# Performance work log

Hardware: AMD Instinct MI355X
Metric: run time of the kernel (lower is better)

## Reference

```python
import jax, jax.numpy as jnp
import numpy as np

H, DH = 8, 64           # heads, dim_head
SCALE = DH ** -0.5


def setup_inputs() -> dict:
    key = jax.random.key(0)
    ks = jax.random.split(key, 8)
    b, f, n, dim = 16, 8, 256, 512
    inner = H * DH
    w = lambda k, s: jax.random.normal(k, s, jnp.float32) * 0.02
    return {
        "x": jax.random.normal(ks[0], (b, f * n, dim), jnp.float32),
        "external": jax.random.normal(ks[1], (b, 1, dim), jnp.float32),
        "Wq": w(ks[2], (dim, inner)), "bq": jnp.zeros((inner,), jnp.float32),
        "Wk": w(ks[3], (dim, inner)), "bk": jnp.zeros((inner,), jnp.float32),
        "Wv": w(ks[4], (dim, inner)), "bv": jnp.zeros((inner,), jnp.float32),
        "Wo": w(ks[5], (inner, dim)), "bo": jnp.zeros((dim,), jnp.float32),
        "f": f,
    }


def reference(x, external, Wq, bq, Wk, bk, Wv, bv, Wo, bo, f):
    b, N, dim = x.shape          # N = f * n
    n = N // f
    xa = jnp.concatenate([external, x], axis=1)          # (b, N+1, dim)

    def proj(W, bias):
        t = xa @ W + bias                                # (b, N+1, H*DH)
        # 'b n (h d) -> (b h) n d'
        return t.reshape(b, N + 1, H, DH).transpose(0, 2, 1, 3).reshape(b * H, N + 1, DH)

    q = proj(Wq, bq) * SCALE
    k = proj(Wk, bk)
    v = proj(Wv, bv)

    def split_local(t):
        ext = jnp.repeat(t[:, :1], f, axis=0)            # (b*H*f, 1, DH)  'b n d -> (b r) n d'
        loc = t[:, 1:].reshape(b * H * f, n, DH)         # 'b (f n) d -> (b f) n d'
        return jnp.concatenate([ext, loc], axis=1)       # (b*H*f, n+1, DH)

    q_, k_, v_ = split_local(q), split_local(k), split_local(v)

    att = jax.nn.softmax(jnp.einsum('bid,bjd->bij', q_, k_), axis=-1)
    out = jnp.einsum('bij,bjd->bid', att, v_)            # (b*H*f, n+1, DH)

    # external token output: '(b h r) d -> b r (h d)' then take r == 1
    ext_out = out[:, 0].reshape(b, H, f, DH).transpose(0, 2, 1, 3).reshape(b, f, H * DH)
    ext_out = ext_out[:, 1:2]                            # (b, 1, H*DH)

    # local outputs: '(b f) n d -> b (f n) d' then '(b h) n d -> b n (h d)'
    main = out[:, 1:].reshape(b, H, N, DH).transpose(0, 2, 1, 3).reshape(b, N, H * DH)

    return main @ Wo + bo, ext_out @ Wo + bo
```

## Files before the change

kernel.cpp:

```cpp
#include <hip/hip_runtime.h>
#include <stdint.h>

#define ATT_SCALE 0.125f

typedef __attribute__((ext_vector_type(8))) short bhalf8;
typedef __attribute__((ext_vector_type(4))) float floatx4;
typedef __attribute__((ext_vector_type(16))) float floatx16;
typedef __attribute__((ext_vector_type(8))) unsigned short ush8;

__device__ __forceinline__ unsigned short f2bf(float f) {
  union { float f; unsigned int u; } v; v.f = f;
  unsigned int r = v.u + 0x7fffu + ((v.u >> 16) & 1u);
  return (unsigned short)(r >> 16);
}
__device__ __forceinline__ float bf2f(unsigned short u) {
  union { unsigned int u; float f; } v; v.u = ((unsigned int)u) << 16;
  return v.f;
}
__device__ __forceinline__ unsigned int pk2(float a, float b) {
  unsigned int r;
  asm("v_cvt_pk_bf16_f32 %0, %1, %2" : "=v"(r) : "v"(a), "v"(b));
  return r;
}
__device__ __forceinline__ void glds16(const void* g, void* l) {
  __builtin_amdgcn_global_load_lds(
      (__attribute__((address_space(1))) void*)g,
      (__attribute__((address_space(3))) void*)l, 16, 0, 0);
}

__global__ __launch_bounds__(256) void k_conv_x(const float* __restrict__ x,
                                                unsigned short* __restrict__ out) {
  int i = blockIdx.x * 256 + threadIdx.x;
  float4 v = ((const float4*)x)[i];
  ((uint2*)out)[i] = make_uint2(pk2(v.x, v.y), pk2(v.z, v.w));
}

__global__ __launch_bounds__(256) void k_conv_w(
    const float* __restrict__ Wq, const float* __restrict__ Wk,
    const float* __restrict__ Wv, const float* __restrict__ Wo,
    const float* __restrict__ bq, const float* __restrict__ bk, const float* __restrict__ bv,
    unsigned short* __restrict__ Wqkvt, unsigned short* __restrict__ Wot,
    float* __restrict__ biasqkv) {
  int idx = blockIdx.x * 256 + threadIdx.x;
  {
    int nn = idx >> 9, k = idx & 511;
    const float* W = (nn < 512) ? Wq : ((nn < 1024) ? Wk : Wv);
    int n = nn & 511;
    Wqkvt[idx] = f2bf(W[k * 512 + n]);
  }
  if (idx < 512 * 512) {
    int n = idx >> 9, k = idx & 511;
    Wot[idx] = f2bf(Wo[k * 512 + n]);
  }
  if (idx < 1536) {
    biasqkv[idx] = (idx < 512) ? bq[idx] : ((idx < 1024) ? bk[idx - 512] : bv[idx - 1024]);
  }
}

__global__ __launch_bounds__(256) void k_ext_qkv(
    const float* __restrict__ ext,
    const float* __restrict__ Wq, const float* __restrict__ Wk, const float* __restrict__ Wv,
    const float* __restrict__ bq, const float* __restrict__ bk, const float* __restrict__ bv,
    float* __restrict__ EQKV) {
  int b = blockIdx.x / 6, c = blockIdx.x % 6;
  int nn = c * 256 + threadIdx.x;
  __shared__ float xs[512];
  xs[threadIdx.x] = ext[b * 512 + threadIdx.x];
  xs[256 + threadIdx.x] = ext[b * 512 + 256 + threadIdx.x];
  __syncthreads();
  const float* W; const float* bias; float scale = 1.f; int n;
  if (nn < 512)      { W = Wq; bias = bq; n = nn;        scale = ATT_SCALE; }
  else if (nn < 1024){ W = Wk; bias = bk; n = nn - 512; }
  else               { W = Wv; bias = bv; n = nn - 1024; }
  float acc = 0.f;
  #pragma unroll 8
  for (int k = 0; k < 512; ++k) acc += xs[k] * W[k * 512 + n];
  EQKV[b * 1536 + nn] = (acc + bias[n]) * scale;
}

template <int EPI>
__global__ __launch_bounds__(256, 2) void k_gemm(
    const unsigned short* __restrict__ A, const unsigned short* __restrict__ B,
    const float* __restrict__ bias, void* __restrict__ Cptr, int N, int nbn) {
  __shared__ __align__(16) unsigned short S[16384];
  int tid = threadIdx.x, lane = tid & 63, wv = tid >> 6;
  int lo = lane & 15, hi = lane >> 4;
  int waveM = wv >> 1, waveN = wv & 1;

  int nwg = gridDim.x;
  int wg = (blockIdx.x & 7) * (nwg >> 3) + (blockIdx.x >> 3);
  int bm = wg / nbn, bn = wg % nbn;

  const unsigned short* Ab = A + (size_t)bm * 128 * 512;
  const unsigned short* Bb = B + (size_t)bn * 128 * 512;
  unsigned short* lA = S;
  unsigned short* lB = S + 8192;

  floatx4 acc[4][4];
  #pragma unroll
  for (int m = 0; m < 4; ++m)
    #pragma unroll
    for (int n = 0; n < 4; ++n) acc[m][n] = floatx4{0.f, 0.f, 0.f, 0.f};

  for (int kt = 0; kt < 8; ++kt) {
    __syncthreads();
    #pragma unroll
    for (int i = 0; i < 4; ++i) {
      int chunk = i * 256 + tid;
      int row = chunk >> 3, slot = chunk & 7;
      glds16(Ab + (size_t)row * 512 + kt * 64 + ((slot ^ (row & 7)) << 3),
             lA + (size_t)(i * 256 + wv * 64) * 8);
    }
    #pragma unroll
    for (int i = 0; i < 4; ++i) {
      int chunk = i * 256 + tid;
      int row = chunk >> 3, slot = chunk & 7;
      glds16(Bb + (size_t)row * 512 + kt * 64 + ((slot ^ (row & 7)) << 3),
             lB + (size_t)(i * 256 + wv * 64) * 8);
    }
    __syncthreads();

    bhalf8 af[4][2], bf4[4][2];
    #pragma unroll
    for (int m = 0; m < 4; ++m) {
      int row = waveM * 64 + m * 16 + lo;
      #pragma unroll
      for (int ks = 0; ks < 2; ++ks)
        af[m][ks] = *(const bhalf8*)(lA + (size_t)row * 64 + (((ks * 4 + hi) ^ (row & 7)) << 3));
    }
    #pragma unroll
    for (int n = 0; n < 4; ++n) {
      int row = waveN * 64 + n * 16 + lo;
      #pragma unroll
      for (int ks = 0; ks < 2; ++ks)
        bf4[n][ks] = *(const bhalf8*)(lB + (size_t)row * 64 + (((ks * 4 + hi) ^ (row & 7)) << 3));
    }
    #pragma unroll
    for (int m = 0; m < 4; ++m)
      #pragma unroll
      for (int n = 0; n < 4; ++n) {
        acc[m][n] = __builtin_amdgcn_mfma_f32_16x16x32_bf16(af[m][0], bf4[n][0], acc[m][n], 0, 0, 0);
        acc[m][n] = __builtin_amdgcn_mfma_f32_16x16x32_bf16(af[m][1], bf4[n][1], acc[m][n], 0, 0, 0);
      }
  }

  #pragma unroll
  for (int m = 0; m < 4; ++m) {
    int row0 = bm * 128 + waveM * 64 + m * 16 + hi * 4;
    #pragma unroll
    for (int n = 0; n < 4; ++n) {
      int col = bn * 128 + waveN * 64 + n * 16 + lo;
      float bb = bias[col];
      #pragma unroll
      for (int r = 0; r < 4; ++r) {
        float v = acc[m][n][r] + bb;
        if constexpr (EPI == 0) {
          if (col < 512) v *= ATT_SCALE;
          ((unsigned short*)Cptr)[(size_t)(row0 + r) * N + col] = f2bf(v);
        } else {
          ((float*)Cptr)[(size_t)(row0 + r) * N + col] = v;
        }
      }
    }
  }
}

#define VTC 296
__global__ __launch_bounds__(512, 4) void k_attn(
    const unsigned short* __restrict__ QKV,
    const float* __restrict__ EQKV,
    unsigned short* __restrict__ mainb) {
  __shared__ __align__(16) unsigned short Ks[288 * 64];
  __shared__ __align__(16) unsigned short Vt[64 * VTC];
  int g = blockIdx.x;
  int b = g >> 6, h = (g >> 3) & 7, j = g & 7;
  int tid = threadIdx.x, lane = tid & 63, wv = tid >> 6;
  int ql = lane & 31, hb = lane >> 5;
  const size_t rowbase = (size_t)b * 2048 + (size_t)j * 256;
  const unsigned short* Kg = QKV + rowbase * 1536 + 512 + h * 64;
  const unsigned short* Vg = QKV + rowbase * 1536 + 1024 + h * 64;

  int qbase = wv * 32;
  const unsigned short* qp = QKV + (rowbase + qbase + ql) * 1536 + h * 64 + hb * 8;
  bhalf8 qf[4];
  #pragma unroll
  for (int c = 0; c < 4; ++c) qf[c] = *(const bhalf8*)(qp + c * 16);

  {
    ush8 z8 = {0, 0, 0, 0, 0, 0, 0, 0};
    for (int c = tid; c < (64 * VTC) / 8; c += 512) ((ush8*)Vt)[c] = z8;
  }
  __syncthreads();

  {
    int keybase = 1 + wv * 32;
    #pragma unroll
    for (int i = 0; i < 4; ++i) {
      int key = keybase + i * 8 + (lane >> 3);
      int slot = lane & 7;
      const unsigned short* src =
          Kg + (size_t)(key - 1) * 1536 + (((slot * 16) ^ ((key & 7) << 4)) >> 1);
      glds16(src, &Ks[(size_t)(keybase + i * 8) * 64]);
    }
  }
  for (int c = tid; c < 2048; c += 512) {
    int key = 1 + (c & 255), d0 = (c >> 8) * 8;
    ush8 vv = *(const ush8*)(Vg + (size_t)(key - 1) * 1536 + d0);
    #pragma unroll
    for (int u = 0; u < 8; ++u) Vt[(d0 + u) * VTC + key] = vv[u];
  }
  if (wv == 0) {
    Ks[lane] = f2bf(EQKV[b * 1536 + 512 + h * 64 + lane]);
    Vt[lane * VTC] = f2bf(EQKV[b * 1536 + 1024 + h * 64 + lane]);
  }
  __syncthreads();

  floatx16 o0, o1;
  #pragma unroll
  for (int i = 0; i < 16; ++i) { o0[i] = 0.f; o1[i] = 0.f; }
  float m = -1e30f, lsum = 0.f;

  #pragma unroll
  for (int t = 0; t < 9; ++t) {
    floatx16 s;
    #pragma unroll
    for (int i = 0; i < 16; ++i) s[i] = 0.f;
    int key = t * 32 + ql;
    __builtin_amdgcn_s_setprio(1);
    #pragma unroll
    for (int c = 0; c < 4; ++c) {
      bhalf8 kf = *(const bhalf8*)((const char*)Ks + key * 128 +
                                   ((c * 32 + hb * 16) ^ ((key & 7) << 4)));
      s = __builtin_amdgcn_mfma_f32_32x32x16_bf16(kf, qf[c], s, 0, 0, 0);
    }
    __builtin_amdgcn_s_setprio(0);
    if (t == 8) {
      #pragma unroll
      for (int r = 0; r < 16; ++r) {
        if (r == 0) { if (hb != 0) s[0] = -1e30f; }
        else s[r] = -1e30f;
      }
    }
    float mt = s[0];
    #pragma unroll
    for (int r = 1; r < 16; ++r) mt = fmaxf(mt, s[r]);
    mt = fmaxf(mt, __shfl_xor(mt, 32, 64));
    if (!__all(mt - m <= 8.f)) {
      float mnew = fmaxf(m, mt);
      float corr = __expf(m - mnew);
      lsum *= corr;
      #pragma unroll
      for (int r = 0; r < 16; ++r) { o0[r] *= corr; o1[r] *= corr; }
      m = mnew;
    }
    float p[16]; float ts = 0.f;
    #pragma unroll
    for (int r = 0; r < 16; ++r) { p[r] = __expf(s[r] - m); ts += p[r]; }
    lsum += ts;
    unsigned int pk[8], qk[8];
    #pragma unroll
    for (int i = 0; i < 8; ++i) pk[i] = pk2(p[2 * i], p[2 * i + 1]);
    #pragma unroll
    for (int i = 0; i < 8; ++i) qk[i] = __shfl_xor(pk[i], 32, 64);
    bhalf8 f0, f1;
    unsigned int* f0u = (unsigned int*)&f0;
    unsigned int* f1u = (unsigned int*)&f1;
    if (hb == 0) {
      f0u[0] = pk[0]; f0u[1] = pk[1]; f0u[2] = qk[0]; f0u[3] = qk[1];
      f1u[0] = pk[4]; f1u[1] = pk[5]; f1u[2] = qk[4]; f1u[3] = qk[5];
    } else {
      f0u[0] = qk[2]; f0u[1] = qk[3]; f0u[2] = pk[2]; f0u[3] = pk[3];
      f1u[0] = qk[6]; f1u[1] = qk[7]; f1u[2] = pk[6]; f1u[3] = pk[7];
    }
    {
      const char* vb0 = (const char*)Vt + ((0 * 32 + ql) * VTC + t * 32 + hb * 8) * 2;
      bhalf8 v0 = *(const bhalf8*)vb0;
      bhalf8 v1 = *(const bhalf8*)(vb0 + 32);
      const char* vb1 = (const char*)Vt + ((1 * 32 + ql) * VTC + t * 32 + hb * 8) * 2;
      bhalf8 w0 = *(const bhalf8*)vb1;
      bhalf8 w1 = *(const bhalf8*)(vb1 + 32);
      __builtin_amdgcn_s_setprio(1);
      o0 = __builtin_amdgcn_mfma_f32_32x32x16_bf16(v0, f0, o0, 0, 0, 0);
      o0 = __builtin_amdgcn_mfma_f32_32x32x16_bf16(v1, f1, o0, 0, 0, 0);
      o1 = __builtin_amdgcn_mfma_f32_32x32x16_bf16(w0, f0, o1, 0, 0, 0);
      o1 = __builtin_amdgcn_mfma_f32_32x32x16_bf16(w1, f1, o1, 0, 0, 0);
      __builtin_amdgcn_s_setprio(0);
    }
  }

  lsum += __shfl_xor(lsum, 32, 64);
  float rinv = 1.f / lsum;
  __syncthreads();
  char* ob = (char*)(Ks + wv * 2048);
  #pragma unroll
  for (int dt = 0; dt < 2; ++dt) {
    #pragma unroll
    for (int i = 0; i < 8; ++i) {
      int d0 = dt * 32 + ((2 * i) & 3) + 8 * (i >> 1) + 4 * hb;
      float a = (dt ? o1[2 * i] : o0[2 * i]) * rinv;
      float c = (dt ? o1[2 * i + 1] : o0[2 * i + 1]) * rinv;
      *(unsigned int*)(ob + ql * 128 + ((d0 * 2) ^ ((ql & 7) << 4))) = pk2(a, c);
    }
  }
  #pragma unroll
  for (int i = 0; i < 4; ++i) {
    int chunk = i * 64 + lane;
    int q = chunk >> 3, slot = chunk & 7;
    bhalf8 vv = *(const bhalf8*)(ob + q * 128 + ((slot * 16) ^ ((q & 7) << 4)));
    *(bhalf8*)(mainb + (rowbase + qbase + q) * 512 + h * 64 + slot * 8) = vv;
  }
}

__global__ __launch_bounds__(256) void k_ext_attn(
    const unsigned short* __restrict__ QKV, const float* __restrict__ EQKV,
    float* __restrict__ extpre) {
  int b = blockIdx.x >> 3, h = blockIdx.x & 7;
  int tid = threadIdx.x, lane = tid & 63, wv = tid >> 6;
  __shared__ float qs[64];
  __shared__ float ps[257];
  __shared__ float red[8];
  __shared__ float acc4[4][64];
  if (tid < 64) qs[tid] = EQKV[b * 1536 + h * 64 + tid];
  __syncthreads();
  const size_t base = (size_t)b * 2048 + 256;
  float sc[2] = {-1e30f, -1e30f};
  #pragma unroll
  for (int it = 0; it < 2; ++it) {
    int key = tid + it * 256;
    if (key < 257) {
      float s = 0.f;
      if (key == 0) {
        const float* kr = EQKV + b * 1536 + 512 + h * 64;
        #pragma unroll 8
        for (int d = 0; d < 64; ++d) s += qs[d] * kr[d];
      } else {
        const unsigned short* kr = QKV + (base + key - 1) * 1536 + 512 + h * 64;
        #pragma unroll
        for (int c = 0; c < 8; ++c) {
          ush8 kv = *(const ush8*)(kr + c * 8);
          #pragma unroll
          for (int u = 0; u < 8; ++u) s += qs[c * 8 + u] * bf2f(kv[u]);
        }
      }
      sc[it] = s;
    }
  }
  float lmax = fmaxf(sc[0], sc[1]);
  for (int d = 1; d < 64; d <<= 1) lmax = fmaxf(lmax, __shfl_xor(lmax, d, 64));
  if (lane == 0) red[wv] = lmax;
  __syncthreads();
  float M = fmaxf(fmaxf(red[0], red[1]), fmaxf(red[2], red[3]));
  float lsum = 0.f;
  #pragma unroll
  for (int it = 0; it < 2; ++it) {
    int key = tid + it * 256;
    if (key < 257) { float p = __expf(sc[it] - M); ps[key] = p; lsum += p; }
  }
  for (int d = 1; d < 64; d <<= 1) lsum += __shfl_xor(lsum, d, 64);
  if (lane == 0) red[4 + wv] = lsum;
  __syncthreads();
  float S = red[4] + red[5] + red[6] + red[7];
  int d = tid & 63, part = tid >> 6;
  float acc = 0.f;
  for (int key = part; key < 257; key += 4) {
    float vv = (key == 0) ? EQKV[b * 1536 + 1024 + h * 64 + d]
                          : bf2f(QKV[(base + key - 1) * 1536 + 1024 + h * 64 + d]);
    acc += ps[key] * vv;
  }
  acc4[part][d] = acc;
  __syncthreads();
  if (tid < 64) {
    float r = (acc4[0][tid] + acc4[1][tid] + acc4[2][tid] + acc4[3][tid]) / S;
    extpre[b * 512 + h * 64 + tid] = r;
  }
}

__global__ __launch_bounds__(256) void k_ext_out(
    const float* __restrict__ extpre, const float* __restrict__ Wo,
    const float* __restrict__ bo, float* __restrict__ out) {
  int b = blockIdx.x, half = blockIdx.y;
  int n = half * 256 + threadIdx.x;
  __shared__ float xs[512];
  xs[threadIdx.x] = extpre[b * 512 + threadIdx.x];
  xs[256 + threadIdx.x] = extpre[b * 512 + 256 + threadIdx.x];
  __syncthreads();
  float acc = bo[n];
  #pragma unroll 8
  for (int k = 0; k < 512; ++k) acc += xs[k] * Wo[k * 512 + n];
  out[16777216 + b * 512 + n] = acc;
}

extern "C" void kernel_launch(void* const* d_in, const int* in_sizes, int n_in,
                              void* d_out, int out_size, void* d_ws, size_t ws_size,
                              hipStream_t stream) {
  (void)in_sizes; (void)n_in; (void)out_size; (void)ws_size;
  const float* x   = (const float*)d_in[0];
  const float* ext = (const float*)d_in[1];
  const float* Wq  = (const float*)d_in[2];
  const float* bq  = (const float*)d_in[3];
  const float* Wk  = (const float*)d_in[4];
  const float* bk  = (const float*)d_in[5];
  const float* Wv  = (const float*)d_in[6];
  const float* bv  = (const float*)d_in[7];
  const float* Wo  = (const float*)d_in[8];
  const float* bo  = (const float*)d_in[9];
  float* out = (float*)d_out;

  char* ws = (char*)d_ws;
  size_t off = 0;
  auto take = [&](size_t bytes) { char* p = ws + off; off += (bytes + 255) & ~(size_t)255; return p; };
  unsigned short* Xbf    = (unsigned short*)take((size_t)32768 * 512 * 2);
  unsigned short* Wqkvt  = (unsigned short*)take((size_t)1536 * 512 * 2);
  unsigned short* Wot    = (unsigned short*)take((size_t)512 * 512 * 2);
  float*          biasqkv= (float*)take(1536 * 4);
  float*          EQKV   = (float*)take(16 * 1536 * 4);
  unsigned short* QKVb   = (unsigned short*)take((size_t)32768 * 1536 * 2);
  unsigned short* mainb  = (unsigned short*)take((size_t)32768 * 512 * 2);
  float*          extpre = (float*)take(16 * 512 * 4);

  k_conv_x<<<16384, 256, 0, stream>>>(x, Xbf);
  k_conv_w<<<3072, 256, 0, stream>>>(Wq, Wk, Wv, Wo, bq, bk, bv, Wqkvt, Wot, biasqkv);
  k_ext_qkv<<<96, 256, 0, stream>>>(ext, Wq, Wk, Wv, bq, bk, bv, EQKV);
  k_gemm<0><<<3072, 256, 0, stream>>>(Xbf, Wqkvt, biasqkv, QKVb, 1536, 12);
  k_attn<<<1024, 512, 0, stream>>>(QKVb, EQKV, mainb);
  k_ext_attn<<<128, 256, 0, stream>>>(QKVb, EQKV, extpre);
  k_gemm<1><<<1024, 256, 0, stream>>>(mainb, Wot, bo, out, 512, 4);
  k_ext_out<<<dim3(16, 2), 256, 0, stream>>>(extpre, Wo, bo, out);
}
```

Measured before the change: 220.7 us.

## Fuse fp32-to-bf16 conversion of x into QKV GEMM; seed attention with external token

Removes the separate k_conv_x pass and its bf16 staging buffer: the QKV GEMM now loads fp32 x tiles straight into LDS with an XOR swizzle and converts them to bf16 in registers before the MFMAs. The attention kernel drops the extra 32-key tile that held the external token. It now computes the external-token score directly in fp32 and uses it to initialise the running max, sum and output, which also removes the Vt zeroing pass and a barrier. The trade-off is that fp32 A tiles double the A-side LDS footprint and load traffic per GEMM tile, and the conversions are repeated by each of the 12 column tiles, which could lower occupancy.

```diff
diff --git a/kernel.cpp b/kernel.cpp
--- a/kernel.cpp
+++ b/kernel.cpp
@@ -26,13 +26,6 @@
   __builtin_amdgcn_global_load_lds(
       (__attribute__((address_space(1))) void*)g,
       (__attribute__((address_space(3))) void*)l, 16, 0, 0);
-}
-
-__global__ __launch_bounds__(256) void k_conv_x(const float* __restrict__ x,
-                                                unsigned short* __restrict__ out) {
-  int i = blockIdx.x * 256 + threadIdx.x;
-  float4 v = ((const float4*)x)[i];
-  ((uint2*)out)[i] = make_uint2(pk2(v.x, v.y), pk2(v.z, v.w));
 }
 
 __global__ __launch_bounds__(256) void k_conv_w(
@@ -78,10 +71,96 @@
   EQKV[b * 1536 + nn] = (acc + bias[n]) * scale;
 }
 
-template <int EPI>
-__global__ __launch_bounds__(256, 2) void k_gemm(
+__global__ __launch_bounds__(256, 2) void k_gemm_qkv(
+    const float* __restrict__ X, const unsigned short* __restrict__ B,
+    const float* __restrict__ bias, unsigned short* __restrict__ C) {
+  __shared__ __align__(16) float Af[8192];
+  __shared__ __align__(16) unsigned short Bs[8192];
+  int tid = threadIdx.x, lane = tid & 63, wv = tid >> 6;
+  int lo = lane & 15, hi = lane >> 4;
+  int waveM = wv >> 1, waveN = wv & 1;
+
+  int nwg = gridDim.x;
+  int wg = (blockIdx.x & 7) * (nwg >> 3) + (blockIdx.x >> 3);
+  int bm = wg / 12, bn = wg % 12;
+
+  const float* Xb = X + (size_t)bm * 128 * 512;
+  const unsigned short* Bb = B + (size_t)bn * 128 * 512;
+
+  floatx4 acc[4][4];
+  #pragma unroll
+  for (int m = 0; m < 4; ++m)
+    #pragma unroll
+    for (int n = 0; n < 4; ++n) acc[m][n] = floatx4{0.f, 0.f, 0.f, 0.f};
+
+  for (int kt = 0; kt < 8; ++kt) {
+    __syncthreads();
+    #pragma unroll
+    for (int i = 0; i < 8; ++i) {
+      int chunk = i * 256 + tid;
+      int row = chunk >> 4, slot = chunk & 15;
+      glds16(Xb + (size_t)row * 512 + kt * 64 + ((slot ^ (row & 15)) << 2),
+             Af + (size_t)(i * 256 + wv * 64) * 4);
+    }
+    #pragma unroll
+    for (int i = 0; i < 4; ++i) {
+      int chunk = i * 256 + tid;
+      int row = chunk >> 3, slot = chunk & 7;
+      glds16(Bb + (size_t)row * 512 + kt * 64 + ((slot ^ (row & 7)) << 3),
+             Bs + (size_t)(i * 256 + wv * 64) * 8);
+    }
+    __syncthreads();
+
+    bhalf8 af[4][2], bf4[4][2];
+    #pragma unroll
+    for (int m = 0; m < 4; ++m) {
+      int row = waveM * 64 + m * 16 + lo;
+      #pragma unroll
+      for (int ks = 0; ks < 2; ++ks) {
+        int j0 = (ks * 4 + hi) * 2;
+        float4 fa = *(const float4*)(Af + (size_t)row * 64 + ((j0 ^ (row & 15)) << 2));
+        float4 fb = *(const float4*)(Af + (size_t)row * 64 + (((j0 + 1) ^ (row & 15)) << 2));
+        unsigned int* w = (unsigned int*)&af[m][ks];
+        w[0] = pk2(fa.x, fa.y); w[1] = pk2(fa.z, fa.w);
+        w[2] = pk2(fb.x, fb.y); w[3] = pk2(fb.z, fb.w);
+      }
+    }
+    #pragma unroll
+    for (int n = 0; n < 4; ++n) {
+      int row = waveN * 64 + n * 16 + lo;
+      #pragma unroll
+      for (int ks = 0; ks < 2; ++ks)
+        bf4[n][ks] = *(const bhalf8*)(Bs + (size_t)row * 64 + (((ks * 4 + hi) ^ (row & 7)) << 3));
+    }
+    #pragma unroll
+    for (int m = 0; m < 4; ++m)
+      #pragma unroll
+      for (int n = 0; n < 4; ++n) {
+        acc[m][n] = __builtin_amdgcn_mfma_f32_16x16x32_bf16(af[m][0], bf4[n][0], acc[m][n], 0, 0, 0);
+        acc[m][n] = __builtin_amdgcn_mfma_f32_16x16x32_bf16(af[m][1], bf4[n][1], acc[m][n], 0, 0, 0);
+      }
+  }
+
+  #pragma unroll
+  for (int m = 0; m < 4; ++m) {
+    int row0 = bm * 128 + waveM * 64 + m * 16 + hi * 4;
+    #pragma unroll
+    for (int n = 0; n < 4; ++n) {
+      int col = bn * 128 + waveN * 64 + n * 16 + lo;
+      float bb = bias[col];
+      #pragma unroll
+      for (int r = 0; r < 4; ++r) {
+        float v = acc[m][n][r] + bb;
+        if (col < 512) v *= ATT_SCALE;
+        C[(size_t)(row0 + r) * 1536 + col] = f2bf(v);
+      }
+    }
+  }
+}
+
+__global__ __launch_bounds__(256, 2) void k_gemm_out(
     const unsigned short* __restrict__ A, const unsigned short* __restrict__ B,
-    const float* __restrict__ bias, void* __restrict__ Cptr, int N, int nbn) {
+    const float* __restrict__ bias, float* __restrict__ C) {
   __shared__ __align__(16) unsigned short S[16384];
   int tid = threadIdx.x, lane = tid & 63, wv = tid >> 6;
   int lo = lane & 15, hi = lane >> 4;
@@ -89,7 +168,7 @@
 
   int nwg = gridDim.x;
   int wg = (blockIdx.x & 7) * (nwg >> 3) + (blockIdx.x >> 3);
-  int bm = wg / nbn, bn = wg % nbn;
+  int bm = wg / 4, bn = wg % 4;
 
   const unsigned short* Ab = A + (size_t)bm * 128 * 512;
   const unsigned short* Bb = B + (size_t)bn * 128 * 512;
@@ -152,15 +231,8 @@
       int col = bn * 128 + waveN * 64 + n * 16 + lo;
       float bb = bias[col];
       #pragma unroll
-      for (int r = 0; r < 4; ++r) {
-        float v = acc[m][n][r] + bb;
-        if constexpr (EPI == 0) {
-          if (col < 512) v *= ATT_SCALE;
-          ((unsigned short*)Cptr)[(size_t)(row0 + r) * N + col] = f2bf(v);
-        } else {
-          ((float*)Cptr)[(size_t)(row0 + r) * N + col] = v;
-        }
-      }
+      for (int r = 0; r < 4; ++r)
+        C[(size_t)(row0 + r) * 512 + col] = acc[m][n][r] + bb;
     }
   }
 }
@@ -170,8 +242,9 @@
     const unsigned short* __restrict__ QKV,
     const float* __restrict__ EQKV,
     unsigned short* __restrict__ mainb) {
-  __shared__ __align__(16) unsigned short Ks[288 * 64];
+  __shared__ __align__(16) unsigned short Ks[256 * 64];
   __shared__ __align__(16) unsigned short Vt[64 * VTC];
+  __shared__ float kx[64], vx[64];
   int g = blockIdx.x;
   int b = g >> 6, h = (g >> 3) & 7, j = g & 7;
   int tid = threadIdx.x, lane = tid & 63, wv = tid >> 6;
@@ -187,41 +260,46 @@
   for (int c = 0; c < 4; ++c) qf[c] = *(const bhalf8*)(qp + c * 16);
 
   {
-    ush8 z8 = {0, 0, 0, 0, 0, 0, 0, 0};
-    for (int c = tid; c < (64 * VTC) / 8; c += 512) ((ush8*)Vt)[c] = z8;
-  }
-  __syncthreads();
-
-  {
-    int keybase = 1 + wv * 32;
+    int keybase = wv * 32;
     #pragma unroll
     for (int i = 0; i < 4; ++i) {
       int key = keybase + i * 8 + (lane >> 3);
       int slot = lane & 7;
       const unsigned short* src =
-          Kg + (size_t)(key - 1) * 1536 + (((slot * 16) ^ ((key & 7) << 4)) >> 1);
+          Kg + (size_t)key * 1536 + (((slot * 16) ^ ((key & 7) << 4)) >> 1);
       glds16(src, &Ks[(size_t)(keybase + i * 8) * 64]);
     }
   }
   for (int c = tid; c < 2048; c += 512) {
-    int key = 1 + (c & 255), d0 = (c >> 8) * 8;
-    ush8 vv = *(const ush8*)(Vg + (size_t)(key - 1) * 1536 + d0);
+    int key = c & 255, d0 = (c >> 8) * 8;
+    ush8 vv = *(const ush8*)(Vg + (size_t)key * 1536 + d0);
     #pragma unroll
     for (int u = 0; u < 8; ++u) Vt[(d0 + u) * VTC + key] = vv[u];
   }
-  if (wv == 0) {
-    Ks[lane] = f2bf(EQKV[b * 1536 + 512 + h * 64 + lane]);
-    Vt[lane * VTC] = f2bf(EQKV[b * 1536 + 1024 + h * 64 + lane]);
-  }
-  __syncthreads();
-
+  if (tid < 64) {
+    kx[tid] = EQKV[b * 1536 + 512 + h * 64 + tid];
+    vx[tid] = EQKV[b * 1536 + 1024 + h * 64 + tid];
+  }
+  __syncthreads();
+
+  float part = 0.f;
+  #pragma unroll
+  for (int c = 0; c < 4; ++c)
+    #pragma unroll
+    for (int u = 0; u < 8; ++u)
+      part += bf2f((unsigned short)qf[c][u]) * kx[c * 16 + hb * 8 + u];
+  float m = part + __shfl_xor(part, 32, 64);
+  float lsum = 1.f;
   floatx16 o0, o1;
   #pragma unroll
-  for (int i = 0; i < 16; ++i) { o0[i] = 0.f; o1[i] = 0.f; }
-  float m = -1e30f, lsum = 0.f;
-
-  #pragma unroll
-  for (int t = 0; t < 9; ++t) {
+  for (int i = 0; i < 8; ++i) {
+    int d0 = ((2 * i) & 3) + 8 * (i >> 1) + 4 * hb;
+    o0[2 * i] = vx[d0];       o0[2 * i + 1] = vx[d0 + 1];
+    o1[2 * i] = vx[32 + d0];  o1[2 * i + 1] = vx[32 + d0 + 1];
+  }
+
+  #pragma unroll
+  for (int t = 0; t < 8; ++t) {
     floatx16 s;
     #pragma unroll
     for (int i = 0; i < 16; ++i) s[i] = 0.f;
@@ -234,13 +312,6 @@
       s = __builtin_amdgcn_mfma_f32_32x32x16_bf16(kf, qf[c], s, 0, 0, 0);
     }
     __builtin_amdgcn_s_setprio(0);
-    if (t == 8) {
-      #pragma unroll
-      for (int r = 0; r < 16; ++r) {
-        if (r == 0) { if (hb != 0) s[0] = -1e30f; }
-        else s[r] = -1e30f;
-      }
-    }
     float mt = s[0];
     #pragma unroll
     for (int r = 1; r < 16; ++r) mt = fmaxf(mt, s[r]);
@@ -409,7 +480,6 @@
   char* ws = (char*)d_ws;
   size_t off = 0;
   auto take = [&](size_t bytes) { char* p = ws + off; off += (bytes + 255) & ~(size_t)255; return p; };
-  unsigned short* Xbf    = (unsigned short*)take((size_t)32768 * 512 * 2);
   unsigned short* Wqkvt  = (unsigned short*)take((size_t)1536 * 512 * 2);
   unsigned short* Wot    = (unsigned short*)take((size_t)512 * 512 * 2);
   float*          biasqkv= (float*)take(1536 * 4);
@@ -418,12 +488,11 @@
   unsigned short* mainb  = (unsigned short*)take((size_t)32768 * 512 * 2);
   float*          extpre = (float*)take(16 * 512 * 4);
 
-  k_conv_x<<<16384, 256, 0, stream>>>(x, Xbf);
   k_conv_w<<<3072, 256, 0, stream>>>(Wq, Wk, Wv, Wo, bq, bk, bv, Wqkvt, Wot, biasqkv);
   k_ext_qkv<<<96, 256, 0, stream>>>(ext, Wq, Wk, Wv, bq, bk, bv, EQKV);
-  k_gemm<0><<<3072, 256, 0, stream>>>(Xbf, Wqkvt, biasqkv, QKVb, 1536, 12);
+  k_gemm_qkv<<<3072, 256, 0, stream>>>(x, Wqkvt, biasqkv, QKVb);
   k_attn<<<1024, 512, 0, stream>>>(QKVb, EQKV, mainb);
   k_ext_attn<<<128, 256, 0, stream>>>(QKVb, EQKV, extpre);
-  k_gemm<1><<<1024, 256, 0, stream>>>(mainb, Wot, bo, out, 512, 4);
+  k_gemm_out<<<1024, 256, 0, stream>>>(mainb, Wot, bo, out);
   k_ext_out<<<dim3(16, 2), 256, 0, stream>>>(extpre, Wo, bo, out);
 }
```

New measurement: 224.6 us. About the same (+1.8%).

## Handle external key/value token analytically instead of a ninth padded tile

Applied to the files above, without the earlier changes.

The external token's key and value are no longer written into shared memory as key slot 0, which had forced a ninth, mostly masked 32-key MFMA tile. The kernel now computes the query-external score with a scalar dot product in fp32 and uses it to seed the online softmax state, with the running max set to that score, the sum set to one and the output initialised to the external value. It also removes the Vt zero-fill pass and one block barrier. The risk is that the hardcoded accumulator layout mapping for the output seed must match the MFMA output layout exactly.

```diff
diff --git a/kernel.cpp b/kernel.cpp
--- a/kernel.cpp
+++ b/kernel.cpp
@@ -170,8 +170,9 @@
     const unsigned short* __restrict__ QKV,
     const float* __restrict__ EQKV,
     unsigned short* __restrict__ mainb) {
-  __shared__ __align__(16) unsigned short Ks[288 * 64];
+  __shared__ __align__(16) unsigned short Ks[256 * 64];
   __shared__ __align__(16) unsigned short Vt[64 * VTC];
+  __shared__ float kx[64], vx[64];
   int g = blockIdx.x;
   int b = g >> 6, h = (g >> 3) & 7, j = g & 7;
   int tid = threadIdx.x, lane = tid & 63, wv = tid >> 6;
@@ -187,41 +188,46 @@
   for (int c = 0; c < 4; ++c) qf[c] = *(const bhalf8*)(qp + c * 16);
 
   {
-    ush8 z8 = {0, 0, 0, 0, 0, 0, 0, 0};
-    for (int c = tid; c < (64 * VTC) / 8; c += 512) ((ush8*)Vt)[c] = z8;
-  }
-  __syncthreads();
-
-  {
-    int keybase = 1 + wv * 32;
+    int keybase = wv * 32;
     #pragma unroll
     for (int i = 0; i < 4; ++i) {
       int key = keybase + i * 8 + (lane >> 3);
       int slot = lane & 7;
       const unsigned short* src =
-          Kg + (size_t)(key - 1) * 1536 + (((slot * 16) ^ ((key & 7) << 4)) >> 1);
+          Kg + (size_t)key * 1536 + (((slot * 16) ^ ((key & 7) << 4)) >> 1);
       glds16(src, &Ks[(size_t)(keybase + i * 8) * 64]);
     }
   }
   for (int c = tid; c < 2048; c += 512) {
-    int key = 1 + (c & 255), d0 = (c >> 8) * 8;
-    ush8 vv = *(const ush8*)(Vg + (size_t)(key - 1) * 1536 + d0);
+    int key = c & 255, d0 = (c >> 8) * 8;
+    ush8 vv = *(const ush8*)(Vg + (size_t)key * 1536 + d0);
     #pragma unroll
     for (int u = 0; u < 8; ++u) Vt[(d0 + u) * VTC + key] = vv[u];
   }
-  if (wv == 0) {
-    Ks[lane] = f2bf(EQKV[b * 1536 + 512 + h * 64 + lane]);
-    Vt[lane * VTC] = f2bf(EQKV[b * 1536 + 1024 + h * 64 + lane]);
-  }
-  __syncthreads();
-
+  if (tid < 64) {
+    kx[tid] = EQKV[b * 1536 + 512 + h * 64 + tid];
+    vx[tid] = EQKV[b * 1536 + 1024 + h * 64 + tid];
+  }
+  __syncthreads();
+
+  float part = 0.f;
+  #pragma unroll
+  for (int c = 0; c < 4; ++c)
+    #pragma unroll
+    for (int u = 0; u < 8; ++u)
+      part += bf2f((unsigned short)qf[c][u]) * kx[c * 16 + hb * 8 + u];
+  float m = part + __shfl_xor(part, 32, 64);
+  float lsum = 1.f;
   floatx16 o0, o1;
   #pragma unroll
-  for (int i = 0; i < 16; ++i) { o0[i] = 0.f; o1[i] = 0.f; }
-  float m = -1e30f, lsum = 0.f;
-
-  #pragma unroll
-  for (int t = 0; t < 9; ++t) {
+  for (int i = 0; i < 8; ++i) {
+    int d0 = ((2 * i) & 3) + 8 * (i >> 1) + 4 * hb;
+    o0[2 * i] = vx[d0];       o0[2 * i + 1] = vx[d0 + 1];
+    o1[2 * i] = vx[32 + d0];  o1[2 * i + 1] = vx[32 + d0 + 1];
+  }
+
+  #pragma unroll
+  for (int t = 0; t < 8; ++t) {
     floatx16 s;
     #pragma unroll
     for (int i = 0; i < 16; ++i) s[i] = 0.f;
@@ -234,13 +240,6 @@
       s = __builtin_amdgcn_mfma_f32_32x32x16_bf16(kf, qf[c], s, 0, 0, 0);
     }
     __builtin_amdgcn_s_setprio(0);
-    if (t == 8) {
-      #pragma unroll
-      for (int r = 0; r < 16; ++r) {
-        if (r == 0) { if (hb != 0) s[0] = -1e30f; }
-        else s[r] = -1e30f;
-      }
-    }
     float mt = s[0];
     #pragma unroll
     for (int r = 1; r < 16; ++r) mt = fmaxf(mt, s[r]);
```

Result: no change. 220.3 us (-0.2%).
